# Kernel tuning notes

Measured on AMD Instinct MI355X. Metric: run time of the kernel, lower is better.

The kernel has to match this reference:

```python
import jax, jax.numpy as jnp
import numpy as np

D_MODEL = 1024
NUM_HEADS = 16
D_K = D_MODEL // NUM_HEADS
B, S = 4, 2048


def setup_inputs() -> dict:
    key = jax.random.key(0)
    ks = jax.random.split(key, 11)
    s = 1.0 / np.sqrt(D_MODEL)  # torch Linear default init scale (uniform bound)
    def lin(k):
        kw, kb = jax.random.split(k)
        W = jax.random.uniform(kw, (D_MODEL, D_MODEL), jnp.float32, -s, s)
        b = jax.random.uniform(kb, (D_MODEL,), jnp.float32, -s, s)
        return W, b
    Wq, bq = lin(ks[0])
    Wk, bk = lin(ks[1])
    Wv, bv = lin(ks[2])
    Wo, bo = lin(ks[3])
    query = jax.random.normal(ks[4], (B, S, D_MODEL), jnp.float32)
    key_t = jax.random.normal(ks[5], (B, S, D_MODEL), jnp.float32)
    value = jax.random.normal(ks[6], (B, S, D_MODEL), jnp.float32)
    mask = jnp.ones((B, 1, 1, S), jnp.int32)
    return {"query": query, "key": key_t, "value": value, "mask": mask,
            "Wq": Wq, "bq": bq, "Wk": Wk, "bk": bk, "Wv": Wv, "bv": bv,
            "Wo": Wo, "bo": bo}


def _split_heads(x):
    # (B, S, D) -> (B, H, S, d_k)
    b, s, _ = x.shape
    return x.reshape(b, s, NUM_HEADS, D_K).transpose(0, 2, 1, 3)


def _mha(query, key, value, mask, Wq, bq, Wk, bk, Wv, bv, Wo, bo):
    Q = _split_heads(query @ Wq.T + bq)
    K = _split_heads(key @ Wk.T + bk)
    V = _split_heads(value @ Wv.T + bv)
    scores = jnp.einsum('bhqd,bhkd->bhqk', Q, K) / np.sqrt(D_K)
    scores = jnp.where(mask == 0, jnp.float32(-1e9), scores)
    attn = jax.nn.softmax(scores, axis=-1)
    out = jnp.einsum('bhqk,bhkd->bhqd', attn, V)  # (B,H,S,d_k)
    out = out.transpose(0, 2, 1, 3).reshape(out.shape[0], out.shape[2], D_MODEL)
    return out @ Wo.T + bo


def reference(query, key, value, mask, Wq, bq, Wk, bk, Wv, bv, Wo, bo):
    return _mha(query, key, value, mask, Wq, bq, Wk, bk, Wv, bv, Wo, bo)
```

## Files before the change

### kernel.cpp

```cpp
#include <hip/hip_runtime.h>


typedef unsigned short u16;
typedef __attribute__((ext_vector_type(8))) short short8;
typedef __attribute__((ext_vector_type(4))) float f32x4;

__device__ __forceinline__ u16 f2bf(float f) {
  union { float f; unsigned int u; } v; v.f = f;
  return (u16)((v.u + 0x7FFFu + ((v.u >> 16) & 1u)) >> 16);
}

__device__ __forceinline__ void gll16(const void* gptr, void* lptr) {
  __builtin_amdgcn_global_load_lds(
      (const __attribute__((address_space(1))) unsigned int*)gptr,
      (__attribute__((address_space(3))) unsigned int*)lptr, 16, 0, 0);
}

__global__ void cvt_x(const float* __restrict__ s, u16* __restrict__ d, int n) {
  const int i = (blockIdx.x * 256 + threadIdx.x) * 8;
  if (i >= n) return;
  f32x4 a = *(const f32x4*)(s + i);
  f32x4 b = *(const f32x4*)(s + i + 4);
  short8 r;
  r[0] = (short)f2bf(a[0]); r[1] = (short)f2bf(a[1]);
  r[2] = (short)f2bf(a[2]); r[3] = (short)f2bf(a[3]);
  r[4] = (short)f2bf(b[0]); r[5] = (short)f2bf(b[1]);
  r[6] = (short)f2bf(b[2]); r[7] = (short)f2bf(b[3]);
  *(short8*)(d + i) = r;
}

__global__ void cvt_w4(const float* __restrict__ w0, const float* __restrict__ w1,
                       const float* __restrict__ w2, const float* __restrict__ w3,
                       u16* __restrict__ d) {
  const int z = blockIdx.y;
  const float* s = (z == 0) ? w0 : (z == 1) ? w1 : (z == 2) ? w2 : w3;
  const int i = (blockIdx.x * 256 + threadIdx.x) * 8;
  u16* dz = d + (size_t)z * 1048576;
  f32x4 a = *(const f32x4*)(s + i);
  f32x4 b = *(const f32x4*)(s + i + 4);
  short8 r;
  r[0] = (short)f2bf(a[0]); r[1] = (short)f2bf(a[1]);
  r[2] = (short)f2bf(a[2]); r[3] = (short)f2bf(a[3]);
  r[4] = (short)f2bf(b[0]); r[5] = (short)f2bf(b[1]);
  r[6] = (short)f2bf(b[2]); r[7] = (short)f2bf(b[3]);
  *(short8*)(dz + i) = r;
}

#define GM 128
#define GN 128
#define GK 32

template <typename TC, bool TRANS>
__global__ __launch_bounds__(256, 3) void gemm_bb(
    const u16* __restrict__ A, const u16* __restrict__ W,
    const float* __restrict__ bias, TC* __restrict__ C,
    int M, int N, int K)
{
  __shared__ __align__(16) u16 As[2][GM * GK];
  __shared__ __align__(16) u16 Bs[2][GN * GK];

  const int tid  = threadIdx.x;
  const int lane = tid & 63;
  const int l15  = lane & 15;
  const int quad = lane >> 4;
  const int wave = tid >> 6;
  const int bm = blockIdx.y * GM;
  const int bn = blockIdx.x * GN;
  const int wm = (wave >> 1) * 64;
  const int wn = (wave & 1) * 64;

  const f32x4 zero4 = {0.f, 0.f, 0.f, 0.f};
  f32x4 acc[4][4];
#pragma unroll
  for (int i = 0; i < 4; i++)
#pragma unroll
    for (int j = 0; j < 4; j++) acc[i][j] = zero4;

  const int srow = tid >> 2;
  const int chl  = (tid & 3) ^ ((tid >> 3) & 3);
  const u16* Ag = A + (size_t)(bm + srow) * K + chl * 8;
  const u16* Wg = W + (size_t)(bn + srow) * K + chl * 8;
  const size_t rowskip = (size_t)64 * K;
  const int chpA = quad ^ ((l15 >> 1) & 3);

  gll16(Ag, &As[0][tid * 8]);
  gll16(Ag + rowskip, &As[0][tid * 8 + 2048]);
  gll16(Wg, &Bs[0][tid * 8]);
  gll16(Wg + rowskip, &Bs[0][tid * 8 + 2048]);

  int buf = 0;
  for (int k0 = 0; k0 < K; k0 += GK) {
    __syncthreads();
    if (k0 + GK < K) {
      const int nb = buf ^ 1;
      gll16(Ag + k0 + GK, &As[nb][tid * 8]);
      gll16(Ag + k0 + GK + rowskip, &As[nb][tid * 8 + 2048]);
      gll16(Wg + k0 + GK, &Bs[nb][tid * 8]);
      gll16(Wg + k0 + GK + rowskip, &Bs[nb][tid * 8 + 2048]);
    }

    short8 af[4], bfr[4];
#pragma unroll
    for (int mi = 0; mi < 4; mi++)
      af[mi] = *(const short8*)&As[buf][(wm + mi * 16 + l15) * GK + chpA * 8];
#pragma unroll
    for (int ni = 0; ni < 4; ni++)
      bfr[ni] = *(const short8*)&Bs[buf][(wn + ni * 16 + l15) * GK + chpA * 8];
#pragma unroll
    for (int mi = 0; mi < 4; mi++)
#pragma unroll
      for (int ni = 0; ni < 4; ni++)
        acc[mi][ni] = __builtin_amdgcn_mfma_f32_16x16x32_bf16(
            af[mi], bfr[ni], acc[mi][ni], 0, 0, 0);
    buf ^= 1;
  }

  float bval[4];
#pragma unroll
  for (int ni = 0; ni < 4; ni++) bval[ni] = bias[bn + wn + ni * 16 + l15];
#pragma unroll
  for (int mi = 0; mi < 4; mi++) {
    const int m0 = bm + wm + mi * 16 + quad * 4;
#pragma unroll
    for (int ni = 0; ni < 4; ni++) {
      const int n = bn + wn + ni * 16 + l15;
      if constexpr (TRANS) {
        ushort4 w;
        w.x = f2bf(acc[mi][ni][0] + bval[ni]);
        w.y = f2bf(acc[mi][ni][1] + bval[ni]);
        w.z = f2bf(acc[mi][ni][2] + bval[ni]);
        w.w = f2bf(acc[mi][ni][3] + bval[ni]);
        *(ushort4*)((u16*)C + (size_t)n * M + m0) = w;
      } else {
#pragma unroll
        for (int r = 0; r < 4; r++) {
          const float v = acc[mi][ni][r] + bval[ni];
          if constexpr (sizeof(TC) == 2)
            C[(size_t)(m0 + r) * N + n] = f2bf(v);
          else
            C[(size_t)(m0 + r) * N + n] = v;
        }
      }
    }
  }
}

__global__ __launch_bounds__(256, 3) void attn_fused(
    const u16* __restrict__ Qb, const u16* __restrict__ Kb,
    const u16* __restrict__ VtG, const int* __restrict__ mask,
    u16* __restrict__ Ob)
{
  constexpr int S = 2048, D = 1024;
  __shared__ __align__(16) u16 Ks[2][64 * 64];
  __shared__ __align__(16) u16 Vs[2][64 * 64];
  __shared__ __align__(16) u16 Pt[4][32 * 64];

  const int tid  = threadIdx.x;
  const int lane = tid & 63;
  const int wave = tid >> 6;
  const int l15  = lane & 15;
  const int quad = lane >> 4;
  const int b = blockIdx.y >> 4;
  const int h = blockIdx.y & 15;
  const int qw = blockIdx.x * 128 + wave * 32;

  const u16* Qp = Qb + (size_t)b * S * D + h * 64;
  const u16* Kp = Kb + (size_t)b * S * D + h * 64;
  const u16* Vg = VtG + (size_t)h * 64 * 8192 + b * 2048;
  const int* mp = mask + b * S;

  short8 qf[2][2];
#pragma unroll
  for (int qb = 0; qb < 2; qb++)
#pragma unroll
    for (int c = 0; c < 2; c++)
      qf[qb][c] = *(const short8*)&Qp[(size_t)(qw + qb * 16 + l15) * D + c * 32 + quad * 8];

  const f32x4 zero4 = {0.f, 0.f, 0.f, 0.f};
  f32x4 o_acc[2][4];
#pragma unroll
  for (int qb = 0; qb < 2; qb++)
#pragma unroll
    for (int ni = 0; ni < 4; ni++) o_acc[qb][ni] = zero4;
  float rsum[2] = {0.f, 0.f};

  const int srow = tid >> 3;
  const int chl  = (tid & 7) ^ (srow & 7);
  const int fsw  = l15 & 7;

#pragma unroll
  for (int p = 0; p < 2; p++) {
    gll16(Kp + (size_t)(p * 32 + srow) * D + chl * 8, &Ks[0][p * 2048 + tid * 8]);
    gll16(Vg + (size_t)(p * 32 + srow) * 8192 + chl * 8, &Vs[0][p * 2048 + tid * 8]);
  }

  f32x4 cm[4];
#pragma unroll
  for (int s = 0; s < 4; s++) {
    int4 mv = *(const int4*)&mp[s * 16 + quad * 4];
    cm[s][0] = mv.x ? 0.f : -1.0e9f;
    cm[s][1] = mv.y ? 0.f : -1.0e9f;
    cm[s][2] = mv.z ? 0.f : -1.0e9f;
    cm[s][3] = mv.w ? 0.f : -1.0e9f;
  }

  constexpr float SCL2 = 0.125f * 1.44269504f;

  int buf = 0;
  for (int kt = 0; kt < S; kt += 64) {
    __syncthreads();

    if (kt + 64 < S) {
      const int nb = buf ^ 1;
#pragma unroll
      for (int p = 0; p < 2; p++) {
        gll16(Kp + (size_t)(kt + 64 + p * 32 + srow) * D + chl * 8,
              &Ks[nb][p * 2048 + tid * 8]);
        gll16(Vg + (size_t)(p * 32 + srow) * 8192 + kt + 64 + chl * 8,
              &Vs[nb][p * 2048 + tid * 8]);
      }
    }
    f32x4 nm[4];
    const int nkt = (kt + 64) & (S - 1);
#pragma unroll
    for (int s = 0; s < 4; s++) {
      int4 mv = *(const int4*)&mp[nkt + s * 16 + quad * 4];
      nm[s][0] = mv.x ? 0.f : -1.0e9f;
      nm[s][1] = mv.y ? 0.f : -1.0e9f;
      nm[s][2] = mv.z ? 0.f : -1.0e9f;
      nm[s][3] = mv.w ? 0.f : -1.0e9f;
    }

    f32x4 sc[2][4];
#pragma unroll
    for (int qb = 0; qb < 2; qb++)
#pragma unroll
      for (int s = 0; s < 4; s++) sc[qb][s] = zero4;
#pragma unroll
    for (int c = 0; c < 2; c++)
#pragma unroll
      for (int s = 0; s < 4; s++) {
        short8 kf = *(const short8*)
            &Ks[buf][(s * 16 + l15) * 64 + ((c * 4 + quad) ^ fsw) * 8];
        sc[0][s] = __builtin_amdgcn_mfma_f32_16x16x32_bf16(kf, qf[0][c], sc[0][s], 0, 0, 0);
        sc[1][s] = __builtin_amdgcn_mfma_f32_16x16x32_bf16(kf, qf[1][c], sc[1][s], 0, 0, 0);
      }

#pragma unroll
    for (int qb = 0; qb < 2; qb++) {
      const int qrow = qb * 16 + l15;
#pragma unroll
      for (int s = 0; s < 4; s++) {
        unsigned int t[4];
#pragma unroll
        for (int r = 0; r < 4; r++) {
          const float sv = fmaf(sc[qb][s][r], SCL2, cm[s][r]);
          const float p = __builtin_amdgcn_exp2f(sv);
          union { float f; unsigned int u; } pu; pu.f = p;
          t[r] = pu.u & 0xffff0000u;
          union { unsigned int u; float f; } tf; tf.u = t[r];
          rsum[qb] += tf.f;
        }
        uint2 w;
        w.x = t[1] | (t[0] >> 16);
        w.y = t[3] | (t[2] >> 16);
        const int phys = (s * 2 + (quad >> 1)) ^ fsw;
        *(uint2*)&Pt[wave][qrow * 64 + phys * 8 + (quad & 1) * 4] = w;
      }
    }

#pragma unroll
    for (int c = 0; c < 2; c++) {
      short8 pf[2];
#pragma unroll
      for (int qb = 0; qb < 2; qb++)
        pf[qb] = *(const short8*)
            &Pt[wave][(qb * 16 + l15) * 64 + ((c * 4 + quad) ^ fsw) * 8];
#pragma unroll
      for (int ni = 0; ni < 4; ni++) {
        short8 vf = *(const short8*)
            &Vs[buf][(ni * 16 + l15) * 64 + ((c * 4 + quad) ^ fsw) * 8];
        o_acc[0][ni] = __builtin_amdgcn_mfma_f32_16x16x32_bf16(pf[0], vf, o_acc[0][ni], 0, 0, 0);
        o_acc[1][ni] = __builtin_amdgcn_mfma_f32_16x16x32_bf16(pf[1], vf, o_acc[1][ni], 0, 0, 0);
      }
    }

#pragma unroll
    for (int s = 0; s < 4; s++) cm[s] = nm[s];
    buf ^= 1;
  }

  float rl[2][4];
#pragma unroll
  for (int qb = 0; qb < 2; qb++) {
    float x = rsum[qb];
    x += __shfl_xor(x, 16, 64);
    x += __shfl_xor(x, 32, 64);
#pragma unroll
    for (int r = 0; r < 4; r++)
      rl[qb][r] = 1.0f / __shfl(x, quad * 4 + r, 64);
  }
#pragma unroll
  for (int qb = 0; qb < 2; qb++) {
    const int q0 = qw + qb * 16 + quad * 4;
#pragma unroll
    for (int ni = 0; ni < 4; ni++)
#pragma unroll
      for (int r = 0; r < 4; r++)
        Ob[(size_t)(b * S + q0 + r) * D + h * 64 + ni * 16 + l15] =
            f2bf(o_acc[qb][ni][r] * rl[qb][r]);
  }
}

extern "C" void kernel_launch(void* const* d_in, const int* in_sizes, int n_in,
                              void* d_out, int out_size, void* d_ws, size_t ws_size,
                              hipStream_t stream) {
  const int M = 8192, N = 1024, K = 1024;
  const float* q    = (const float*)d_in[0];
  const float* k    = (const float*)d_in[1];
  const float* v    = (const float*)d_in[2];
  const int*   mask = (const int*)d_in[3];
  const float* Wq = (const float*)d_in[4];
  const float* bq = (const float*)d_in[5];
  const float* Wk = (const float*)d_in[6];
  const float* bk = (const float*)d_in[7];
  const float* Wv = (const float*)d_in[8];
  const float* bv = (const float*)d_in[9];
  const float* Wo = (const float*)d_in[10];
  const float* bo = (const float*)d_in[11];

  const size_t MN = (size_t)M * N;
  u16* Qb  = (u16*)d_ws;
  u16* Kb  = Qb + MN;
  u16* VtG = Kb + MN;
  u16* Ob  = VtG + MN;
  u16* Wc  = Ob + MN;

  dim3 bb(256);
  dim3 gg(N / GN, M / GM);
  const int xblk = M * N / (256 * 8);

  cvt_w4<<<dim3(512, 4), bb, 0, stream>>>(Wq, Wk, Wv, Wo, Wc);

  cvt_x<<<xblk, bb, 0, stream>>>(q, Ob, M * N);
  gemm_bb<u16, false><<<gg, bb, 0, stream>>>(Ob, Wc + 0 * 1048576, bq, Qb, M, N, K);
  cvt_x<<<xblk, bb, 0, stream>>>(k, Ob, M * N);
  gemm_bb<u16, false><<<gg, bb, 0, stream>>>(Ob, Wc + 1 * 1048576, bk, Kb, M, N, K);
  cvt_x<<<xblk, bb, 0, stream>>>(v, Ob, M * N);
  gemm_bb<u16, true><<<gg, bb, 0, stream>>>(Ob, Wc + 2 * 1048576, bv, VtG, M, N, K);

  attn_fused<<<dim3(16, 64), bb, 0, stream>>>(Qb, Kb, VtG, mask, Ob);

  gemm_bb<float, false><<<gg, bb, 0, stream>>>(Ob, Wc + 3 * 1048576, bo, (float*)d_out, M, N, K);
}
```

Before: 391.8 us.

## Batch QKV projections into one launch and move softmax row-sum onto MFMA

Replaces the three separate input-conversion kernels and Q/K/V GEMMs with one batched conversion kernel and one batched GEMM over a z-grid, when the workspace is large enough. This gives the GPU more concurrent blocks and removes launch gaps. The softmax scale and log2e factor are folded into the Q projection epilogue, which drops an FMA per score. The row sums of P are now computed with an MFMA against a vector of ones instead of scalar adds and cross-lane shuffles. The batched path needs a larger workspace and keeps the old path as a fallback.

```diff
diff --git a/kernel.cpp b/kernel.cpp
--- a/kernel.cpp
+++ b/kernel.cpp
@@ -27,6 +27,22 @@
   r[4] = (short)f2bf(b[0]); r[5] = (short)f2bf(b[1]);
   r[6] = (short)f2bf(b[2]); r[7] = (short)f2bf(b[3]);
   *(short8*)(d + i) = r;
+}
+
+__global__ void cvt_x3(const float* __restrict__ q, const float* __restrict__ k,
+                       const float* __restrict__ v, u16* __restrict__ d) {
+  const int z = blockIdx.y;
+  const float* s = (z == 0) ? q : (z == 1) ? k : v;
+  const int i = (blockIdx.x * 256 + threadIdx.x) * 8;
+  u16* dz = d + (size_t)z * 8388608;
+  f32x4 a = *(const f32x4*)(s + i);
+  f32x4 b = *(const f32x4*)(s + i + 4);
+  short8 r;
+  r[0] = (short)f2bf(a[0]); r[1] = (short)f2bf(a[1]);
+  r[2] = (short)f2bf(a[2]); r[3] = (short)f2bf(a[3]);
+  r[4] = (short)f2bf(b[0]); r[5] = (short)f2bf(b[1]);
+  r[6] = (short)f2bf(b[2]); r[7] = (short)f2bf(b[3]);
+  *(short8*)(dz + i) = r;
 }
 
 __global__ void cvt_w4(const float* __restrict__ w0, const float* __restrict__ w1,
@@ -54,7 +70,7 @@
 __global__ __launch_bounds__(256, 3) void gemm_bb(
     const u16* __restrict__ A, const u16* __restrict__ W,
     const float* __restrict__ bias, TC* __restrict__ C,
-    int M, int N, int K)
+    int M, int N, int K, float scale)
 {
   __shared__ __align__(16) u16 As[2][GM * GK];
   __shared__ __align__(16) u16 Bs[2][GN * GK];
@@ -126,20 +142,119 @@
       const int n = bn + wn + ni * 16 + l15;
       if constexpr (TRANS) {
         ushort4 w;
-        w.x = f2bf(acc[mi][ni][0] + bval[ni]);
-        w.y = f2bf(acc[mi][ni][1] + bval[ni]);
-        w.z = f2bf(acc[mi][ni][2] + bval[ni]);
-        w.w = f2bf(acc[mi][ni][3] + bval[ni]);
+        w.x = f2bf((acc[mi][ni][0] + bval[ni]) * scale);
+        w.y = f2bf((acc[mi][ni][1] + bval[ni]) * scale);
+        w.z = f2bf((acc[mi][ni][2] + bval[ni]) * scale);
+        w.w = f2bf((acc[mi][ni][3] + bval[ni]) * scale);
         *(ushort4*)((u16*)C + (size_t)n * M + m0) = w;
       } else {
 #pragma unroll
         for (int r = 0; r < 4; r++) {
-          const float v = acc[mi][ni][r] + bval[ni];
+          const float v = (acc[mi][ni][r] + bval[ni]) * scale;
           if constexpr (sizeof(TC) == 2)
             C[(size_t)(m0 + r) * N + n] = f2bf(v);
           else
             C[(size_t)(m0 + r) * N + n] = v;
         }
+      }
+    }
+  }
+}
+
+__global__ __launch_bounds__(256, 3) void gemm_qkv(
+    const u16* __restrict__ Ab, const u16* __restrict__ Wc,
+    const float* __restrict__ bq, const float* __restrict__ bk,
+    const float* __restrict__ bv, u16* __restrict__ Qo,
+    u16* __restrict__ Ko, u16* __restrict__ Vo, float qscale)
+{
+  const int M = 8192, N = 1024, K = 1024;
+  const int z = blockIdx.z;
+  const u16* A = Ab + (size_t)z * 8388608;
+  const u16* W = Wc + (size_t)z * 1048576;
+  const float* bias = (z == 0) ? bq : (z == 1) ? bk : bv;
+  u16* C = (z == 0) ? Qo : (z == 1) ? Ko : Vo;
+  const float scale = (z == 0) ? qscale : 1.0f;
+  const bool trans = (z == 2);
+
+  __shared__ __align__(16) u16 As[2][GM * GK];
+  __shared__ __align__(16) u16 Bs[2][GN * GK];
+
+  const int tid  = threadIdx.x;
+  const int lane = tid & 63;
+  const int l15  = lane & 15;
+  const int quad = lane >> 4;
+  const int wave = tid >> 6;
+  const int bm = blockIdx.y * GM;
+  const int bn = blockIdx.x * GN;
+  const int wm = (wave >> 1) * 64;
+  const int wn = (wave & 1) * 64;
+
+  const f32x4 zero4 = {0.f, 0.f, 0.f, 0.f};
+  f32x4 acc[4][4];
+#pragma unroll
+  for (int i = 0; i < 4; i++)
+#pragma unroll
+    for (int j = 0; j < 4; j++) acc[i][j] = zero4;
+
+  const int srow = tid >> 2;
+  const int chl  = (tid & 3) ^ ((tid >> 3) & 3);
+  const u16* Ag = A + (size_t)(bm + srow) * K + chl * 8;
+  const u16* Wg = W + (size_t)(bn + srow) * K + chl * 8;
+  const size_t rowskip = (size_t)64 * K;
+  const int chpA = quad ^ ((l15 >> 1) & 3);
+
+  gll16(Ag, &As[0][tid * 8]);
+  gll16(Ag + rowskip, &As[0][tid * 8 + 2048]);
+  gll16(Wg, &Bs[0][tid * 8]);
+  gll16(Wg + rowskip, &Bs[0][tid * 8 + 2048]);
+
+  int buf = 0;
+  for (int k0 = 0; k0 < K; k0 += GK) {
+    __syncthreads();
+    if (k0 + GK < K) {
+      const int nb = buf ^ 1;
+      gll16(Ag + k0 + GK, &As[nb][tid * 8]);
+      gll16(Ag + k0 + GK + rowskip, &As[nb][tid * 8 + 2048]);
+      gll16(Wg + k0 + GK, &Bs[nb][tid * 8]);
+      gll16(Wg + k0 + GK + rowskip, &Bs[nb][tid * 8 + 2048]);
+    }
+
+    short8 af[4], bfr[4];
+#pragma unroll
+    for (int mi = 0; mi < 4; mi++)
+      af[mi] = *(const short8*)&As[buf][(wm + mi * 16 + l15) * GK + chpA * 8];
+#pragma unroll
+    for (int ni = 0; ni < 4; ni++)
+      bfr[ni] = *(const short8*)&Bs[buf][(wn + ni * 16 + l15) * GK + chpA * 8];
+#pragma unroll
+    for (int mi = 0; mi < 4; mi++)
+#pragma unroll
+      for (int ni = 0; ni < 4; ni++)
+        acc[mi][ni] = __builtin_amdgcn_mfma_f32_16x16x32_bf16(
+            af[mi], bfr[ni], acc[mi][ni], 0, 0, 0);
+    buf ^= 1;
+  }
+
+  float bval[4];
+#pragma unroll
+  for (int ni = 0; ni < 4; ni++) bval[ni] = bias[bn + wn + ni * 16 + l15];
+#pragma unroll
+  for (int mi = 0; mi < 4; mi++) {
+    const int m0 = bm + wm + mi * 16 + quad * 4;
+#pragma unroll
+    for (int ni = 0; ni < 4; ni++) {
+      const int n = bn + wn + ni * 16 + l15;
+      if (trans) {
+        ushort4 w;
+        w.x = f2bf(acc[mi][ni][0] + bval[ni]);
+        w.y = f2bf(acc[mi][ni][1] + bval[ni]);
+        w.z = f2bf(acc[mi][ni][2] + bval[ni]);
+        w.w = f2bf(acc[mi][ni][3] + bval[ni]);
+        *(ushort4*)(C + (size_t)n * M + m0) = w;
+      } else {
+#pragma unroll
+        for (int r = 0; r < 4; r++)
+          C[(size_t)(m0 + r) * N + n] = f2bf((acc[mi][ni][r] + bval[ni]) * scale);
       }
     }
   }
@@ -182,7 +297,10 @@
   for (int qb = 0; qb < 2; qb++)
 #pragma unroll
     for (int ni = 0; ni < 4; ni++) o_acc[qb][ni] = zero4;
-  float rsum[2] = {0.f, 0.f};
+  f32x4 l_acc[2] = {zero4, zero4};
+
+  const short8 one8 = {(short)0x3f80, (short)0x3f80, (short)0x3f80, (short)0x3f80,
+                       (short)0x3f80, (short)0x3f80, (short)0x3f80, (short)0x3f80};
 
   const int srow = tid >> 3;
   const int chl  = (tid & 7) ^ (srow & 7);
@@ -204,8 +322,6 @@
     cm[s][3] = mv.w ? 0.f : -1.0e9f;
   }
 
-  constexpr float SCL2 = 0.125f * 1.44269504f;
-
   int buf = 0;
   for (int kt = 0; kt < S; kt += 64) {
     __syncthreads();
@@ -254,16 +370,13 @@
         unsigned int t[4];
 #pragma unroll
         for (int r = 0; r < 4; r++) {
-          const float sv = fmaf(sc[qb][s][r], SCL2, cm[s][r]);
-          const float p = __builtin_amdgcn_exp2f(sv);
-          union { float f; unsigned int u; } pu; pu.f = p;
-          t[r] = pu.u & 0xffff0000u;
-          union { unsigned int u; float f; } tf; tf.u = t[r];
-          rsum[qb] += tf.f;
+          union { float f; unsigned int u; } pu;
+          pu.f = __builtin_amdgcn_exp2f(sc[qb][s][r] + cm[s][r]);
+          t[r] = pu.u;
         }
         uint2 w;
-        w.x = t[1] | (t[0] >> 16);
-        w.y = t[3] | (t[2] >> 16);
+        w.x = __builtin_amdgcn_perm(t[1], t[0], 0x07060302u);
+        w.y = __builtin_amdgcn_perm(t[3], t[2], 0x07060302u);
         const int phys = (s * 2 + (quad >> 1)) ^ fsw;
         *(uint2*)&Pt[wave][qrow * 64 + phys * 8 + (quad & 1) * 4] = w;
       }
@@ -276,6 +389,8 @@
       for (int qb = 0; qb < 2; qb++)
         pf[qb] = *(const short8*)
             &Pt[wave][(qb * 16 + l15) * 64 + ((c * 4 + quad) ^ fsw) * 8];
+      l_acc[0] = __builtin_amdgcn_mfma_f32_16x16x32_bf16(pf[0], one8, l_acc[0], 0, 0, 0);
+      l_acc[1] = __builtin_amdgcn_mfma_f32_16x16x32_bf16(pf[1], one8, l_acc[1], 0, 0, 0);
 #pragma unroll
       for (int ni = 0; ni < 4; ni++) {
         short8 vf = *(const short8*)
@@ -292,14 +407,9 @@
 
   float rl[2][4];
 #pragma unroll
-  for (int qb = 0; qb < 2; qb++) {
-    float x = rsum[qb];
-    x += __shfl_xor(x, 16, 64);
-    x += __shfl_xor(x, 32, 64);
-#pragma unroll
-    for (int r = 0; r < 4; r++)
-      rl[qb][r] = 1.0f / __shfl(x, quad * 4 + r, 64);
-  }
+  for (int qb = 0; qb < 2; qb++)
+#pragma unroll
+    for (int r = 0; r < 4; r++) rl[qb][r] = 1.0f / l_acc[qb][r];
 #pragma unroll
   for (int qb = 0; qb < 2; qb++) {
     const int q0 = qw + qb * 16 + quad * 4;
@@ -330,26 +440,46 @@
   const float* bo = (const float*)d_in[11];
 
   const size_t MN = (size_t)M * N;
-  u16* Qb  = (u16*)d_ws;
-  u16* Kb  = Qb + MN;
-  u16* VtG = Kb + MN;
-  u16* Ob  = VtG + MN;
-  u16* Wc  = Ob + MN;
+  const float QSC = 0.125f * 1.44269504f;
 
   dim3 bb(256);
   dim3 gg(N / GN, M / GM);
-  const int xblk = M * N / (256 * 8);
-
-  cvt_w4<<<dim3(512, 4), bb, 0, stream>>>(Wq, Wk, Wv, Wo, Wc);
-
-  cvt_x<<<xblk, bb, 0, stream>>>(q, Ob, M * N);
-  gemm_bb<u16, false><<<gg, bb, 0, stream>>>(Ob, Wc + 0 * 1048576, bq, Qb, M, N, K);
-  cvt_x<<<xblk, bb, 0, stream>>>(k, Ob, M * N);
-  gemm_bb<u16, false><<<gg, bb, 0, stream>>>(Ob, Wc + 1 * 1048576, bk, Kb, M, N, K);
-  cvt_x<<<xblk, bb, 0, stream>>>(v, Ob, M * N);
-  gemm_bb<u16, true><<<gg, bb, 0, stream>>>(Ob, Wc + 2 * 1048576, bv, VtG, M, N, K);
-
-  attn_fused<<<dim3(16, 64), bb, 0, stream>>>(Qb, Kb, VtG, mask, Ob);
-
-  gemm_bb<float, false><<<gg, bb, 0, stream>>>(Ob, Wc + 3 * 1048576, bo, (float*)d_out, M, N, K);
-}
+
+  const size_t need_batched = (6 * MN + 4 * 1048576) * sizeof(u16);
+  if (ws_size >= need_batched) {
+    u16* Ax  = (u16*)d_ws;
+    u16* Qb  = Ax + 3 * MN;
+    u16* Kb  = Ax + 4 * MN;
+    u16* VtG = Ax + 5 * MN;
+    u16* Wc  = Ax + 6 * MN;
+    u16* Ob  = Ax;
+
+    cvt_w4<<<dim3(512, 4), bb, 0, stream>>>(Wq, Wk, Wv, Wo, Wc);
+    cvt_x3<<<dim3(4096, 3), bb, 0, stream>>>(q, k, v, Ax);
+    gemm_qkv<<<dim3(8, 64, 3), bb, 0, stream>>>(Ax, Wc, bq, bk, bv, Qb, Kb, VtG, QSC);
+    attn_fused<<<dim3(16, 64), bb, 0, stream>>>(Qb, Kb, VtG, mask, Ob);
+    gemm_bb<float, false><<<gg, bb, 0, stream>>>(Ob, Wc + 3 * 1048576, bo,
+                                                 (float*)d_out, M, N, K, 1.0f);
+  } else {
+    u16* Qb  = (u16*)d_ws;
+    u16* Kb  = Qb + MN;
+    u16* VtG = Kb + MN;
+    u16* Ob  = VtG + MN;
+    u16* Wc  = Ob + MN;
+    const int xblk = (int)(MN / (256 * 8));
+
+    cvt_w4<<<dim3(512, 4), bb, 0, stream>>>(Wq, Wk, Wv, Wo, Wc);
+
+    cvt_x<<<xblk, bb, 0, stream>>>(q, Ob, M * N);
+    gemm_bb<u16, false><<<gg, bb, 0, stream>>>(Ob, Wc + 0 * 1048576, bq, Qb, M, N, K, QSC);
+    cvt_x<<<xblk, bb, 0, stream>>>(k, Ob, M * N);
+    gemm_bb<u16, false><<<gg, bb, 0, stream>>>(Ob, Wc + 1 * 1048576, bk, Kb, M, N, K, 1.0f);
+    cvt_x<<<xblk, bb, 0, stream>>>(v, Ob, M * N);
+    gemm_bb<u16, true><<<gg, bb, 0, stream>>>(Ob, Wc + 2 * 1048576, bv, VtG, M, N, K, 1.0f);
+
+    attn_fused<<<dim3(16, 64), bb, 0, stream>>>(Qb, Kb, VtG, mask, Ob);
+
+    gemm_bb<float, false><<<gg, bb, 0, stream>>>(Ob, Wc + 3 * 1048576, bo,
+                                                 (float*)d_out, M, N, K, 1.0f);
+  }
+}
```

Result: no change. 385.0 us (-1.7%).
